# Performance work log

Hardware: AMD Instinct MI355X
Metric: run time of the kernel (lower is better)

Reference implementation:

```python
import jax, jax.numpy as jnp
import numpy as np

KERNEL_SIZES = [1, 2, 3]
KERNEL_NUM = 11
SIGMA = 0.1
EXACT_SIGMA = 0.001
EMBED_DIM = 300
HIDDEN = 128
Q_VOCAB = 30000
D_VOCAB = 30000


def _mus_sigmas():
    mus, sigmas = [], []
    K = KERNEL_NUM
    for i in range(K):
        mu = 1.0 / (K - 1) + 2.0 * i / (K - 1) - 1.0
        sigma = SIGMA
        if mu > 1.0:
            sigma = EXACT_SIGMA
            mu = 1.0
        mus.append(mu)
        sigmas.append(sigma)
    return jnp.asarray(mus, jnp.float32), jnp.asarray(sigmas, jnp.float32)


def _conv_tanh(x_bcl, w, b, ks):
    # x_bcl: (B, C_in, L); ConstantPad1d((0, ks)) + Conv1d(kernel=ks+1) keeps length L
    y = jax.lax.conv_general_dilated(
        x_bcl, w, window_strides=(1,), padding=[(0, ks)],
        dimension_numbers=('NCW', 'OIW', 'NCW'))
    return jnp.tanh(y + b[None, :, None])  # (B, H, L)


def _l2norm(x):
    n = jnp.sqrt(jnp.sum(x * x, axis=-1, keepdims=True))
    return x / jnp.maximum(n, 1e-12)


def setup_inputs() -> dict:
    key = jax.random.key(0)
    ks = jax.random.split(key, 16)
    inp = {
        'query': jax.random.randint(ks[0], (128, 128), 0, Q_VOCAB),
        'doc': jax.random.randint(ks[1], (128, 512), 0, D_VOCAB),
        'q_emb': jax.random.normal(ks[2], (Q_VOCAB, EMBED_DIM), jnp.float32) * 0.1,
        'd_emb': jax.random.normal(ks[3], (D_VOCAB, EMBED_DIM), jnp.float32) * 0.1,
        'out_w': jax.random.normal(ks[4], (1, 3 * 3 * KERNEL_NUM), jnp.float32) * 0.1,
        'out_b': jnp.zeros((1,), jnp.float32),
    }
    for idx, k in enumerate(KERNEL_SIZES):
        fan_in = EMBED_DIM * (k + 1)
        inp[f'conv_w{idx}'] = jax.random.normal(ks[5 + 2 * idx], (HIDDEN, EMBED_DIM, k + 1), jnp.float32) / np.sqrt(fan_in)
        inp[f'conv_b{idx}'] = jnp.zeros((HIDDEN,), jnp.float32)
    return inp


def reference(query, doc, q_emb, d_emb, conv_w0, conv_b0, conv_w1, conv_b1,
              conv_w2, conv_b2, out_w, out_b):
    mus, sigmas = _mus_sigmas()
    inv2s2 = 1.0 / (2.0 * sigmas * sigmas)  # (K,)

    q_e = q_emb[query].transpose(0, 2, 1)  # (B, D, Lq)
    d_e = d_emb[doc].transpose(0, 2, 1)    # (B, D, Ld)

    cws = [(conv_w0, conv_b0), (conv_w1, conv_b1), (conv_w2, conv_b2)]
    # q_convs/d_convs share weights (same nn.Sequential appended to both lists)
    q_convs = [_l2norm(_conv_tanh(q_e, w, b, ks).transpose(0, 2, 1))
               for (w, b), ks in zip(cws, KERNEL_SIZES)]  # each (B, Lq, H)
    d_convs = [_l2norm(_conv_tanh(d_e, w, b, ks).transpose(0, 2, 1))
               for (w, b), ks in zip(cws, KERNEL_SIZES)]  # each (B, Ld, H)

    KM = []
    for qi in range(3):
        for di in range(3):
            mm = jnp.einsum('bld,brd->blr', q_convs[qi], d_convs[di])  # (B,Lq,Ld)
            # Gaussian kernel soft-histogram, vectorized over all kernels
            kern = jnp.exp(-(mm[..., None] - mus) ** 2 * inv2s2)  # (B,Lq,Ld,K)
            K = jnp.log1p(kern.sum(axis=2)).sum(axis=1)           # (B,K)
            KM.append(K)
    phi = jnp.concatenate(KM, axis=1)  # (B, 9*KERNEL_NUM)
    return phi @ out_w.T + out_b       # (B, 1)
```

## Files before the change

### kernel.cpp

```cpp
#include <hip/hip_runtime.h>
#include <hip/hip_bf16.h>

typedef __hip_bfloat16 bf16;
typedef __attribute__((ext_vector_type(8))) short short8;
typedef __attribute__((ext_vector_type(4))) float f32x4;

#define NB 128
#define NH 128
#define NLQ 128
#define NLD 512
#define NEMB 300
#define XQROWS 132
#define XDROWS 516
#define XCOLS 320

__device__ __forceinline__ unsigned short bfbits(float x) {
    __hip_bfloat16 h = __float2bfloat16(x);
    return *reinterpret_cast<unsigned short*>(&h);
}

__device__ __forceinline__ float fast_tanh(float x) {
    x = fminf(9.f, fmaxf(-9.f, x));
    float e = __builtin_amdgcn_exp2f(x * 2.8853900817779268f);
    return (e - 1.f) * __builtin_amdgcn_rcpf(e + 1.f);
}

__global__ void pack_w(const float* __restrict__ cw0, const float* __restrict__ cw1,
                       const float* __restrict__ cw2, bf16* __restrict__ Wp)
{
    int widx = blockIdx.y;
    int W = widx + 2;
    int e = blockIdx.x * 256 + threadIdx.x;
    if (e >= W * 40960) return;
    int ch = e >> 12;
    int cc = ch / W;
    int t  = ch - cc * W;
    int h  = (e >> 5) & 127;
    int cp = e & 31;
    int c  = cc * 32 + cp;
    const float* cw = (widx == 0) ? cw0 : (widx == 1 ? cw1 : cw2);
    float v = (c < NEMB) ? cw[(h * NEMB + c) * W + t] : 0.f;
    size_t off = (widx == 0) ? 0 : (widx == 1 ? 81920 : 204800);
    Wp[off + e] = __float2bfloat16(v);
}

__global__ __launch_bounds__(256)
void pack_x(const int* __restrict__ q_tok, const int* __restrict__ d_tok,
            const float* __restrict__ q_emb, const float* __restrict__ d_emb,
            bf16* __restrict__ Xq, bf16* __restrict__ Xd)
{
    int gid = blockIdx.x * 256 + threadIdx.x;
    int row = gid / 20, g = gid - row * 20;
    const float* emb; bf16* dst; int tok;
    if (row < NB * XQROWS) {
        int b = row / XQROWS, l = row - b * XQROWS;
        tok = (l < NLQ) ? q_tok[b * NLQ + l] : -1;
        emb = q_emb;
        dst = Xq + (size_t)row * XCOLS + g * 16;
    } else {
        int rowd = row - NB * XQROWS;
        int b = rowd / XDROWS, l = rowd - b * XDROWS;
        tok = (l < NLD) ? d_tok[b * NLD + l] : -1;
        emb = d_emb;
        dst = Xd + (size_t)rowd * XCOLS + g * 16;
    }
    int c0 = g * 16;
    float4 v[4];
    #pragma unroll
    for (int q = 0; q < 4; ++q) {
        int c = c0 + q * 4;
        v[q] = make_float4(0.f, 0.f, 0.f, 0.f);
        if (tok >= 0 && c < NEMB)
            v[q] = *reinterpret_cast<const float4*>(emb + (size_t)tok * NEMB + c);
    }
    short8 o0, o1;
    o0[0] = (short)bfbits(v[0].x); o0[1] = (short)bfbits(v[0].y);
    o0[2] = (short)bfbits(v[0].z); o0[3] = (short)bfbits(v[0].w);
    o0[4] = (short)bfbits(v[1].x); o0[5] = (short)bfbits(v[1].y);
    o0[6] = (short)bfbits(v[1].z); o0[7] = (short)bfbits(v[1].w);
    o1[0] = (short)bfbits(v[2].x); o1[1] = (short)bfbits(v[2].y);
    o1[2] = (short)bfbits(v[2].z); o1[3] = (short)bfbits(v[2].w);
    o1[4] = (short)bfbits(v[3].x); o1[5] = (short)bfbits(v[3].y);
    o1[6] = (short)bfbits(v[3].z); o1[7] = (short)bfbits(v[3].w);
    *reinterpret_cast<short8*>(dst) = o0;
    *reinterpret_cast<short8*>(dst + 8) = o1;
}

__global__ __launch_bounds__(512, 4)
void conv_kernel(const bf16* __restrict__ Xq, const bf16* __restrict__ Xd,
                 const bf16* __restrict__ Wp,
                 const float* __restrict__ cb0, const float* __restrict__ cb1,
                 const float* __restrict__ cb2,
                 bf16* __restrict__ qn, bf16* __restrict__ dn)
{
    __shared__ bf16 Xs[2][132][40];
    __shared__ float ssq[2][256];

    int bx = blockIdx.x;
    int widx = bx % 3;
    int inner = bx / 3;
    int W = widx + 2;
    const bf16* wp = Wp + ((widx == 0) ? 0 : (widx == 1 ? 81920 : 204800));
    const float* cb = (widx == 0) ? cb0 : (widx == 1 ? cb1 : cb2);

    int tid = threadIdx.x;
    int lane = tid & 63;
    int wv = tid >> 6;
    int wr = wv >> 1;
    int wc = wv & 1;
    int s_wave = wr >> 1;
    int lr_base = (wr & 1) * 64;

    bf16* outp; int L;
    int sb0, sb1, sl00, sl01;
    const bf16* xbase;
    size_t grow0, grow1;
    if (inner < 64) {
        outp = qn + (size_t)widx * NB * NLQ * NH;
        L = NLQ; sb0 = inner * 2; sb1 = sb0 + 1; sl00 = 0; sl01 = 0;
        xbase = Xq; grow0 = (size_t)sb0 * XQROWS; grow1 = (size_t)sb1 * XQROWS;
    } else {
        int i = inner - 64;
        outp = dn + (size_t)widx * NB * NLD * NH;
        L = NLD; sb0 = i >> 1; sb1 = sb0; sl00 = (i & 1) * 256; sl01 = sl00 + 128;
        xbase = Xd; grow0 = (size_t)sb0 * XDROWS + sl00; grow1 = grow0 + 128;
    }

    int sr = tid >> 2;
    int colg = tid & 3;
    const bf16* gsrc0 = xbase + (grow0 + sr) * XCOLS + colg * 8;
    const bf16* gsrc1 = xbase + (grow1 + sr) * XCOLS + colg * 8;
    bf16* ld0 = &Xs[0][sr][colg * 8];
    bf16* ld1 = &Xs[1][sr][colg * 8];
    bool has_tail = (tid >= 448 && tid < 480);
    int j = tid - 448;
    int ts = (j >> 2) >> 2, trr = 128 + ((j >> 2) & 3), tcolg = j & 3;
    const bf16* gsrcT = xbase + ((ts ? grow1 : grow0) + trr) * XCOLS + tcolg * 8;
    bf16* ldT = &Xs[ts][trr][tcolg * 8];

    short8 a0, a1, at;
    a0 = *reinterpret_cast<const short8*>(gsrc0);
    a1 = *reinterpret_cast<const short8*>(gsrc1);
    if (has_tail) at = *reinterpret_cast<const short8*>(gsrcT);
    *reinterpret_cast<short8*>(ld0) = a0;
    *reinterpret_cast<short8*>(ld1) = a1;
    if (has_tail) *reinterpret_cast<short8*>(ldT) = at;
    __syncthreads();

    f32x4 acc[4][4];
    #pragma unroll
    for (int m = 0; m < 4; ++m)
        #pragma unroll
        for (int n = 0; n < 4; ++n)
            acc[m][n] = (f32x4){0.f, 0.f, 0.f, 0.f};

    const bf16* pB = wp + ((size_t)((wc * 64 + (lane & 15)) * 4 + (lane >> 4))) * 8;

    int step = 0;
    for (int cc = 0; cc < 10; ++cc) {
        if (cc < 9) {
            a0 = *reinterpret_cast<const short8*>(gsrc0 + (cc + 1) * 32);
            a1 = *reinterpret_cast<const short8*>(gsrc1 + (cc + 1) * 32);
            if (has_tail) at = *reinterpret_cast<const short8*>(gsrcT + (cc + 1) * 32);
        }
        for (int t = 0; t < W; ++t, ++step) {
            const bf16* pBs = pB + (size_t)step * 4096;
            short8 bv[4], af[4];
            #pragma unroll
            for (int n = 0; n < 4; ++n)
                bv[n] = *reinterpret_cast<const short8*>(pBs + n * 512);
            #pragma unroll
            for (int m = 0; m < 4; ++m)
                af[m] = *reinterpret_cast<const short8*>(
                    &Xs[s_wave][lr_base + m * 16 + (lane & 15) + t][(lane >> 4) * 8]);
            #pragma unroll
            for (int m = 0; m < 4; ++m)
                #pragma unroll
                for (int n = 0; n < 4; ++n)
                    acc[m][n] = __builtin_amdgcn_mfma_f32_16x16x32_bf16(af[m], bv[n], acc[m][n], 0, 0, 0);
        }
        if (cc < 9) {
            __syncthreads();
            *reinterpret_cast<short8*>(ld0) = a0;
            *reinterpret_cast<short8*>(ld1) = a1;
            if (has_tail) *reinterpret_cast<short8*>(ldT) = at;
            __syncthreads();
        }
    }

    float ssl[4][4];
    #pragma unroll
    for (int m = 0; m < 4; ++m)
        #pragma unroll
        for (int i = 0; i < 4; ++i) ssl[m][i] = 0.f;

    #pragma unroll
    for (int n = 0; n < 4; ++n) {
        float bias = cb[wc * 64 + n * 16 + (lane & 15)];
        #pragma unroll
        for (int m = 0; m < 4; ++m)
            #pragma unroll
            for (int i = 0; i < 4; ++i) {
                float v = fast_tanh(acc[m][n][i] + bias);
                acc[m][n][i] = v;
                ssl[m][i] += v * v;
            }
    }
    #pragma unroll
    for (int m = 0; m < 4; ++m)
        #pragma unroll
        for (int i = 0; i < 4; ++i) {
            float s = ssl[m][i];
            s += __shfl_xor(s, 1); s += __shfl_xor(s, 2);
            s += __shfl_xor(s, 4); s += __shfl_xor(s, 8);
            ssl[m][i] = s;
        }
    if ((lane & 15) == 0) {
        #pragma unroll
        for (int m = 0; m < 4; ++m)
            #pragma unroll
            for (int i = 0; i < 4; ++i)
                ssq[wc][wr * 64 + m * 16 + (lane >> 4) * 4 + i] = ssl[m][i];
    }
    __syncthreads();
    #pragma unroll
    for (int m = 0; m < 4; ++m)
        #pragma unroll
        for (int i = 0; i < 4; ++i) {
            int r = wr * 64 + m * 16 + (lane >> 4) * 4 + i;
            float s2 = ssq[0][r] + ssq[1][r];
            float sc = 1.f / fmaxf(sqrtf(s2), 1e-12f);
            int s = r >> 7, lr = r & 127;
            int b = s ? sb1 : sb0;
            int l = (s ? sl01 : sl00) + lr;
            bf16* dst = outp + ((size_t)(b * L + l)) * NH;
            #pragma unroll
            for (int n = 0; n < 4; ++n)
                dst[wc * 64 + n * 16 + (lane & 15)] = __float2bfloat16(acc[m][n][i] * sc);
        }
}

__global__ __launch_bounds__(512, 5)
void sim_kernel(const bf16* __restrict__ qn, const bf16* __restrict__ dn,
                float* __restrict__ phi)
{
    __shared__ bf16 Qs[128][136];
    __shared__ bf16 Ds[64][136];
    __shared__ float wsum[2][11];
    float (*red)[128][11] = reinterpret_cast<float(*)[128][11]>(&Ds[0][0]);

    int blk = blockIdx.x;
    int b = blk / 9;
    int pair = blk - b * 9;
    int qi = pair / 3, di = pair - qi * 3;

    int tid = threadIdx.x, lane = tid & 63, wv = tid >> 6;
    int wr = wv >> 2;
    int wc = wv & 3;

    const bf16* qbase = qn + ((size_t)qi * NB + b) * (NLQ * NH);
    const bf16* dbase = dn + ((size_t)di * NB + b) * (NLD * NH);

    {
        int r = tid >> 2, h0 = (tid & 3) * 32;
        #pragma unroll
        for (int v = 0; v < 4; ++v)
            *reinterpret_cast<short8*>(&Qs[r][h0 + v * 8]) =
                *reinterpret_cast<const short8*>(qbase + (size_t)r * NH + h0 + v * 8);
    }

    int dr = tid >> 3, dc = (tid & 7) * 16;
    {
        short8 st[2];
        #pragma unroll
        for (int v = 0; v < 2; ++v)
            st[v] = *reinterpret_cast<const short8*>(dbase + (size_t)dr * NH + dc + v * 8);
        #pragma unroll
        for (int v = 0; v < 2; ++v)
            *reinterpret_cast<short8*>(&Ds[dr][dc + v * 8]) = st[v];
    }
    __syncthreads();

    float sums[2][11];
    #pragma unroll
    for (int n = 0; n < 2; ++n)
        #pragma unroll
        for (int k = 0; k < 11; ++k) sums[n][k] = 0.f;

    const float C1 = 1.8315638888734179e-2f;
    const float C2 = 3.3546262790251185e-4f;
    const float C3 = 6.1442123533282098e-6f;
    const float C4 = 1.1253517471925912e-7f;

    for (int cc = 0; cc < 8; ++cc) {
        f32x4 acc[2][2];
        #pragma unroll
        for (int m = 0; m < 2; ++m)
            #pragma unroll
            for (int n = 0; n < 2; ++n)
                acc[m][n] = (f32x4){0.f, 0.f, 0.f, 0.f};

        #pragma unroll
        for (int kc = 0; kc < 4; ++kc) {
            short8 af[2], bq[2];
            #pragma unroll
            for (int m = 0; m < 2; ++m)
                af[m] = *reinterpret_cast<const short8*>(
                    &Ds[wr * 32 + m * 16 + (lane & 15)][kc * 32 + (lane >> 4) * 8]);
            #pragma unroll
            for (int n = 0; n < 2; ++n)
                bq[n] = *reinterpret_cast<const short8*>(
                    &Qs[wc * 32 + n * 16 + (lane & 15)][kc * 32 + (lane >> 4) * 8]);
            #pragma unroll
            for (int m = 0; m < 2; ++m)
                #pragma unroll
                for (int n = 0; n < 2; ++n)
                    acc[m][n] = __builtin_amdgcn_mfma_f32_16x16x32_bf16(af[m], bq[n], acc[m][n], 0, 0, 0);
        }
        __syncthreads();

        short8 st[2];
        if (cc < 7) {
            #pragma unroll
            for (int v = 0; v < 2; ++v)
                st[v] = *reinterpret_cast<const short8*>(
                    dbase + (size_t)((cc + 1) * 64 + dr) * NH + dc + v * 8);
        }

        #pragma unroll
        for (int n = 0; n < 2; ++n)
            #pragma unroll
            for (int m = 0; m < 2; ++m)
                #pragma unroll
                for (int i = 0; i < 4; ++i) {
                    float x = acc[m][n][i];
                    float R  = __builtin_amdgcn_exp2f(x * 28.853900817779268f);
                    float Ri = __builtin_amdgcn_exp2f(x * -28.853900817779268f);
                    float d4 = x + 0.1f;
                    float E4 = __builtin_amdgcn_exp2f(d4 * d4 * -72.134752044448169f);
                    sums[n][4] += E4;
                    float u = E4 * R;        sums[n][5] += u;
                    u *= R; u *= C1;         sums[n][6] += u;
                    u *= R; u *= C2;         sums[n][7] += u;
                    u *= R; u *= C3;         sums[n][8] += u;
                    u *= R; u *= C4;         sums[n][9] += u;
                    float w = E4 * Ri; w *= C1; sums[n][3] += w;
                    w *= Ri; w *= C2;        sums[n][2] += w;
                    w *= Ri; w *= C3;        sums[n][1] += w;
                    w *= Ri; w *= C4;        sums[n][0] += w;
                    float d1 = x - 1.0f;
                    sums[n][10] += __builtin_amdgcn_exp2f(d1 * d1 * -721347.52044448f);
                }

        if (cc < 7) {
            #pragma unroll
            for (int v = 0; v < 2; ++v)
                *reinterpret_cast<short8*>(&Ds[dr][dc + v * 8]) = st[v];
            __syncthreads();
        }
    }

    #pragma unroll
    for (int n = 0; n < 2; ++n)
        #pragma unroll
        for (int k = 0; k < 11; ++k) {
            float s = sums[n][k];
            s += __shfl_xor(s, 16);
            s += __shfl_xor(s, 32);
            sums[n][k] = s;
        }
    if ((lane >> 4) == 0) {
        #pragma unroll
        for (int n = 0; n < 2; ++n)
            #pragma unroll
            for (int k = 0; k < 11; ++k)
                red[wr][wc * 32 + n * 16 + (lane & 15)][k] = sums[n][k];
    }
    __syncthreads();
    if (tid < 128) {
        float lv[11];
        #pragma unroll
        for (int k = 0; k < 11; ++k)
            lv[k] = log1pf(red[0][tid][k] + red[1][tid][k]);
        #pragma unroll
        for (int k = 0; k < 11; ++k) {
            float s = lv[k];
            s += __shfl_xor(s, 1); s += __shfl_xor(s, 2); s += __shfl_xor(s, 4);
            s += __shfl_xor(s, 8); s += __shfl_xor(s, 16); s += __shfl_xor(s, 32);
            lv[k] = s;
        }
        if ((tid & 63) == 0) {
            #pragma unroll
            for (int k = 0; k < 11; ++k) wsum[tid >> 6][k] = lv[k];
        }
    }
    __syncthreads();
    if (tid < 11) phi[b * 99 + pair * 11 + tid] = wsum[0][tid] + wsum[1][tid];
}

__global__ void final_kernel(const float* __restrict__ phi, const float* __restrict__ ow,
                             const float* __restrict__ obias, float* __restrict__ out)
{
    int b = threadIdx.x;
    float s = obias[0];
    #pragma unroll
    for (int j = 0; j < 99; ++j) s += phi[b * 99 + j] * ow[j];
    out[b] = s;
}

extern "C" void kernel_launch(void* const* d_in, const int* in_sizes, int n_in,
                              void* d_out, int out_size, void* d_ws, size_t ws_size,
                              hipStream_t stream)
{
    const int*   query = (const int*)d_in[0];
    const int*   doc   = (const int*)d_in[1];
    const float* q_emb = (const float*)d_in[2];
    const float* d_emb = (const float*)d_in[3];
    const float* out_w = (const float*)d_in[4];
    const float* out_b = (const float*)d_in[5];
    const float* cw0 = (const float*)d_in[6];
    const float* cb0 = (const float*)d_in[7];
    const float* cw1 = (const float*)d_in[8];
    const float* cb1 = (const float*)d_in[9];
    const float* cw2 = (const float*)d_in[10];
    const float* cb2 = (const float*)d_in[11];

    const size_t QN = (size_t)NB * NLQ * NH;
    const size_t DN = (size_t)NB * NLD * NH;
    const size_t XQN = (size_t)NB * XQROWS * XCOLS;
    const size_t XDN = (size_t)NB * XDROWS * XCOLS;

    bf16* Wp = (bf16*)d_ws;
    bf16* Xq = Wp + 368640;
    bf16* Xd = Xq + XQN;
    bf16* qn = Xd + XDN;
    bf16* dn = qn + 3 * QN;
    float* phi = (float*)(dn + 3 * DN);

    pack_w<<<dim3(640, 3), 256, 0, stream>>>(cw0, cw1, cw2, Wp);
    pack_x<<<6480, 256, 0, stream>>>(query, doc, q_emb, d_emb, Xq, Xd);
    conv_kernel<<<960, 512, 0, stream>>>(Xq, Xd, Wp, cb0, cb1, cb2, qn, dn);
    sim_kernel<<<NB * 9, 512, 0, stream>>>(qn, dn, phi);
    final_kernel<<<1, 128, 0, stream>>>(phi, out_w, out_b, (float*)d_out);
}
```

Baseline: 254.7 us.

## Pack Gaussian kernel math into float2, replace exp with rcp, skip exact-match exp

The Gaussian soft-histogram epilogue now processes two MFMA outputs at once as float2 vectors, so the compiler can emit packed FP32 ops on MI355X. The second exp2 for the negative ratio becomes a reciprocal of the first. The exact-match kernel's exp is now evaluated only when some lane in the wavefront has a similarity above 0.98, since below that threshold the narrow sigma term underflows. Launch bounds drop from 5 to 4 blocks per CU to give the compiler more registers for the wider accumulators, which may lower occupancy.

```diff
diff --git a/kernel.cpp b/kernel.cpp
--- a/kernel.cpp
+++ b/kernel.cpp
@@ -4,6 +4,7 @@
 typedef __hip_bfloat16 bf16;
 typedef __attribute__((ext_vector_type(8))) short short8;
 typedef __attribute__((ext_vector_type(4))) float f32x4;
+typedef __attribute__((ext_vector_type(2))) float f32x2;
 
 #define NB 128
 #define NH 128
@@ -240,7 +241,7 @@
         }
 }
 
-__global__ __launch_bounds__(512, 5)
+__global__ __launch_bounds__(512, 4)
 void sim_kernel(const bf16* __restrict__ qn, const bf16* __restrict__ dn,
                 float* __restrict__ phi)
 {
@@ -281,11 +282,11 @@
     }
     __syncthreads();
 
-    float sums[2][11];
+    f32x2 sums2[2][11];
     #pragma unroll
     for (int n = 0; n < 2; ++n)
         #pragma unroll
-        for (int k = 0; k < 11; ++k) sums[n][k] = 0.f;
+        for (int k = 0; k < 11; ++k) sums2[n][k] = (f32x2){0.f, 0.f};
 
     const float C1 = 1.8315638888734179e-2f;
     const float C2 = 3.3546262790251185e-4f;
@@ -330,27 +331,40 @@
         #pragma unroll
         for (int n = 0; n < 2; ++n)
             #pragma unroll
-            for (int m = 0; m < 2; ++m)
-                #pragma unroll
-                for (int i = 0; i < 4; ++i) {
-                    float x = acc[m][n][i];
-                    float R  = __builtin_amdgcn_exp2f(x * 28.853900817779268f);
-                    float Ri = __builtin_amdgcn_exp2f(x * -28.853900817779268f);
-                    float d4 = x + 0.1f;
-                    float E4 = __builtin_amdgcn_exp2f(d4 * d4 * -72.134752044448169f);
-                    sums[n][4] += E4;
-                    float u = E4 * R;        sums[n][5] += u;
-                    u *= R; u *= C1;         sums[n][6] += u;
-                    u *= R; u *= C2;         sums[n][7] += u;
-                    u *= R; u *= C3;         sums[n][8] += u;
-                    u *= R; u *= C4;         sums[n][9] += u;
-                    float w = E4 * Ri; w *= C1; sums[n][3] += w;
-                    w *= Ri; w *= C2;        sums[n][2] += w;
-                    w *= Ri; w *= C3;        sums[n][1] += w;
-                    w *= Ri; w *= C4;        sums[n][0] += w;
-                    float d1 = x - 1.0f;
-                    sums[n][10] += __builtin_amdgcn_exp2f(d1 * d1 * -721347.52044448f);
+            for (int i = 0; i < 4; ++i) {
+                f32x2 x2;
+                x2.x = acc[0][n][i];
+                x2.y = acc[1][n][i];
+                f32x2 ax = x2 * 28.853900817779268f;
+                f32x2 R, Ri, E4;
+                R.x = __builtin_amdgcn_exp2f(ax.x);
+                R.y = __builtin_amdgcn_exp2f(ax.y);
+                Ri.x = __builtin_amdgcn_rcpf(R.x);
+                Ri.y = __builtin_amdgcn_rcpf(R.y);
+                f32x2 d4 = x2 + 0.1f;
+                f32x2 t = d4 * d4 * (-72.134752044448169f);
+                E4.x = __builtin_amdgcn_exp2f(t.x);
+                E4.y = __builtin_amdgcn_exp2f(t.y);
+                sums2[n][4] += E4;
+                f32x2 u = E4 * R;
+                sums2[n][5] += u;
+                u *= R; u *= C1; sums2[n][6] += u;
+                u *= R; u *= C2; sums2[n][7] += u;
+                u *= R; u *= C3; sums2[n][8] += u;
+                u *= R; u *= C4; sums2[n][9] += u;
+                f32x2 w = E4 * Ri; w *= C1; sums2[n][3] += w;
+                w *= Ri; w *= C2; sums2[n][2] += w;
+                w *= Ri; w *= C3; sums2[n][1] += w;
+                w *= Ri; w *= C4; sums2[n][0] += w;
+                if (__any(fmaxf(x2.x, x2.y) > 0.98f)) {
+                    f32x2 d1 = x2 - 1.0f;
+                    f32x2 t1 = d1 * d1 * (-721347.52044448f);
+                    f32x2 e;
+                    e.x = __builtin_amdgcn_exp2f(t1.x);
+                    e.y = __builtin_amdgcn_exp2f(t1.y);
+                    sums2[n][10] += e;
                 }
+            }
 
         if (cc < 7) {
             #pragma unroll
@@ -364,17 +378,17 @@
     for (int n = 0; n < 2; ++n)
         #pragma unroll
         for (int k = 0; k < 11; ++k) {
-            float s = sums[n][k];
+            float s = sums2[n][k].x + sums2[n][k].y;
             s += __shfl_xor(s, 16);
             s += __shfl_xor(s, 32);
-            sums[n][k] = s;
+            sums2[n][k].x = s;
         }
     if ((lane >> 4) == 0) {
         #pragma unroll
         for (int n = 0; n < 2; ++n)
             #pragma unroll
             for (int k = 0; k < 11; ++k)
-                red[wr][wc * 32 + n * 16 + (lane & 15)][k] = sums[n][k];
+                red[wr][wc * 32 + n * 16 + (lane & 15)][k] = sums2[n][k].x;
     }
     __syncthreads();
     if (tid < 128) {
```

After: 227.9 us. 10.5% less time.
